# Kernel tuning notes

Measured on AMD Instinct MI355X. Metric: run time of the kernel, lower is better.

Reference implementation:

```python
import jax, jax.numpy as jnp
import numpy as np

POOLED = 7          # output_size
SCALE = 0.25        # spatial_scale
SRATIO = 2          # sampling_ratio (fixed in module)
IMG_H, IMG_W = 800.0, 1216.0


def setup_inputs() -> dict:
    key = jax.random.key(0)
    kf, kb, kx, ky, kw, kh = jax.random.split(key, 6)
    B, C, H, W = 2, 256, 200, 304
    features = jax.random.normal(kf, (B, C, H, W), dtype=jnp.float32)
    N = 1000
    bidx = jax.random.randint(kb, (N,), 0, B).astype(jnp.float32)
    x1 = jax.random.uniform(kx, (N,), minval=0.0, maxval=IMG_W - 32.0)
    y1 = jax.random.uniform(ky, (N,), minval=0.0, maxval=IMG_H - 32.0)
    bw = jax.random.uniform(kw, (N,), minval=16.0, maxval=256.0)
    bh = jax.random.uniform(kh, (N,), minval=16.0, maxval=256.0)
    x2 = jnp.minimum(x1 + bw, IMG_W)
    y2 = jnp.minimum(y1 + bh, IMG_H)
    rois = jnp.stack([bidx, x1, y1, x2, y2], axis=1).astype(jnp.float32)
    return {"features": features, "rois": rois}


def _axis_interp(c, size):
    """Per-axis bilinear prep, matching torchvision roi_align (aligned=False)."""
    valid = (c >= -1.0) & (c <= size)
    c = jnp.maximum(c, 0.0)
    lo = jnp.floor(c).astype(jnp.int32)
    at_edge = lo >= size - 1
    lo = jnp.minimum(lo, size - 1)
    hi = jnp.minimum(lo + 1, size - 1)
    c = jnp.where(at_edge, lo.astype(c.dtype), c)
    frac = c - lo.astype(c.dtype)
    return lo, hi, frac, valid


def reference(features, rois):
    B, C, H, W = features.shape
    N = rois.shape[0]
    P, s = POOLED, SRATIO
    Ps = P * s

    f = jnp.transpose(features, (0, 2, 3, 1))  # [B, H, W, C]
    b = rois[:, 0].astype(jnp.int32)
    x1 = rois[:, 1] * SCALE
    y1 = rois[:, 2] * SCALE
    x2 = rois[:, 3] * SCALE
    y2 = rois[:, 4] * SCALE
    roi_w = jnp.maximum(x2 - x1, 1.0)
    roi_h = jnp.maximum(y2 - y1, 1.0)
    bin_w = roi_w / P
    bin_h = roi_h / P

    # sample-point centers: ph*bin + (iy+0.5)*bin/s  ==  (idx+0.5)/s * bin
    off = (jnp.arange(Ps, dtype=jnp.float32) + 0.5) / s  # [Ps]
    ys = y1[:, None] + off[None, :] * bin_h[:, None]     # [N, Ps]
    xs = x1[:, None] + off[None, :] * bin_w[:, None]     # [N, Ps]

    yl, yh, ly, vy = _axis_interp(ys, H)
    xl, xh, lx, vx = _axis_interp(xs, W)
    hy, hx = 1.0 - ly, 1.0 - lx

    bb = b[:, None, None]
    YL, YH = yl[:, :, None], yh[:, :, None]
    XL, XH = xl[:, None, :], xh[:, None, :]
    # gathered corner values: [N, Ps, Ps, C]
    v11 = f[bb, YL, XL]
    v12 = f[bb, YL, XH]
    v21 = f[bb, YH, XL]
    v22 = f[bb, YH, XH]

    w11 = (hy[:, :, None] * hx[:, None, :])[..., None]
    w12 = (hy[:, :, None] * lx[:, None, :])[..., None]
    w21 = (ly[:, :, None] * hx[:, None, :])[..., None]
    w22 = (ly[:, :, None] * lx[:, None, :])[..., None]
    mask = (vy[:, :, None] & vx[:, None, :]).astype(f.dtype)[..., None]

    val = (w11 * v11 + w12 * v12 + w21 * v21 + w22 * v22) * mask  # [N,Ps,Ps,C]
    out = val.reshape(N, P, s, P, s, C).mean(axis=(2, 4))          # [N,P,P,C]
    return jnp.transpose(out, (0, 3, 1, 2))                        # [N,C,P,P]
```

## Files before the change

### kernel.cpp

```cpp
#include <hip/hip_runtime.h>
#include <hip/hip_fp16.h>

#define POOLED 7
#define PP 49
#define ROI_SCALE 0.25f
#define FH 200
#define FW 304
#define FHW 60800
#define FC 256

__global__ __launch_bounds__(256) void transpose_f16(
    const float* __restrict__ in, __half* __restrict__ out)
{
    __shared__ float tile[64][33];
    const int b   = blockIdx.z;
    const int hw0 = blockIdx.x * 32;
    const int c0  = blockIdx.y * 64;
    const int tx  = threadIdx.x;
    const int ty  = threadIdx.y;

    #pragma unroll
    for (int i = 0; i < 8; i++) {
        int c = c0 + ty + i * 8;
        tile[ty + i * 8][tx] = in[((size_t)b * FC + c) * FHW + hw0 + tx];
    }
    __syncthreads();
    #pragma unroll
    for (int i = 0; i < 4; i++) {
        int hwl = ty + i * 8;
        __half2 h = __floats2half2_rn(tile[2 * tx][hwl], tile[2 * tx + 1][hwl]);
        *reinterpret_cast<__half2*>(
            out + ((size_t)b * FHW + hw0 + hwl) * FC + c0 + 2 * tx) = h;
    }
}

__device__ __forceinline__ float4 ldpx(const __half* p) {
    uint2 u = *reinterpret_cast<const uint2*>(p);
    __half2 h0 = *reinterpret_cast<const __half2*>(&u.x);
    __half2 h1 = *reinterpret_cast<const __half2*>(&u.y);
    float2 f0 = __half22float2(h0);
    float2 f1 = __half22float2(h1);
    return make_float4(f0.x, f0.y, f1.x, f1.y);
}

__global__ __launch_bounds__(256) void roi_gather_f16(
    const __half* __restrict__ f,
    const float* __restrict__ rois,
    float* __restrict__ out)
{
    __shared__ float s_out[FC * 13];
    __shared__ int   s_ylo[14], s_yhi[14], s_xlo[14], s_xhi[14];
    __shared__ float s_ly[14], s_lx[14];
    __shared__ int   s_vy[14], s_vx[14];

    const int n    = blockIdx.x;
    const int q    = blockIdx.y;
    const int b0   = q * 13;
    const int nb   = (q == 3) ? 10 : 13;
    const int tid  = threadIdx.x;
    const int lane = tid & 63;
    const int wave = tid >> 6;

    const float* r = rois + (size_t)n * 5;
    const int   bi = (int)r[0];
    const float x1 = r[1] * ROI_SCALE;
    const float y1 = r[2] * ROI_SCALE;
    const float bin_w = fmaxf(r[3] * ROI_SCALE - x1, 1.0f) / (float)POOLED;
    const float bin_h = fmaxf(r[4] * ROI_SCALE - y1, 1.0f) / (float)POOLED;

    if (tid < 14) {
        float c = y1 + ((float)tid + 0.5f) * 0.5f * bin_h;
        int v = (c >= -1.0f) && (c <= (float)FH);
        c = fmaxf(c, 0.0f);
        int lo = (int)floorf(c);
        int edge = (lo >= FH - 1);
        lo = min(lo, FH - 1);
        s_yhi[tid] = min(lo + 1, FH - 1);
        s_ylo[tid] = lo;
        s_ly[tid]  = edge ? 0.0f : (c - (float)lo);
        s_vy[tid]  = v;
    } else if (tid >= 64 && tid < 78) {
        int j = tid - 64;
        float c = x1 + ((float)j + 0.5f) * 0.5f * bin_w;
        int v = (c >= -1.0f) && (c <= (float)FW);
        c = fmaxf(c, 0.0f);
        int lo = (int)floorf(c);
        int edge = (lo >= FW - 1);
        lo = min(lo, FW - 1);
        s_xhi[j] = min(lo + 1, FW - 1);
        s_xlo[j] = lo;
        s_lx[j]  = edge ? 0.0f : (c - (float)lo);
        s_vx[j]  = v;
    }
    __syncthreads();

    const __half* fb = f + (size_t)bi * (FHW * FC) + 4 * lane;

    for (int bin = b0 + wave; bin < b0 + nb; bin += 4) {
        int ph = bin / 7, pw = bin - ph * 7;
        float ax = 0.f, ay = 0.f, az = 0.f, aw = 0.f;
        #pragma unroll
        for (int iy = 0; iy < 2; iy++) {
            int   sy = 2 * ph + iy;
            int   rlo = s_ylo[sy] * FW, rhi = s_yhi[sy] * FW;
            float ly = s_ly[sy], hy = 1.0f - ly;
            float my = s_vy[sy] ? 1.0f : 0.0f;
            #pragma unroll
            for (int ix = 0; ix < 2; ix++) {
                int   sx = 2 * pw + ix;
                int   xlo = s_xlo[sx], xhi = s_xhi[sx];
                float lx = s_lx[sx], hx = 1.0f - lx;
                float m = s_vx[sx] ? my : 0.0f;
                float w11 = m * hy * hx, w12 = m * hy * lx;
                float w21 = m * ly * hx, w22 = m * ly * lx;
                float4 v11 = ldpx(fb + (size_t)(rlo + xlo) * FC);
                float4 v12 = ldpx(fb + (size_t)(rlo + xhi) * FC);
                float4 v21 = ldpx(fb + (size_t)(rhi + xlo) * FC);
                float4 v22 = ldpx(fb + (size_t)(rhi + xhi) * FC);
                ax += w11 * v11.x + w12 * v12.x + w21 * v21.x + w22 * v22.x;
                ay += w11 * v11.y + w12 * v12.y + w21 * v21.y + w22 * v22.y;
                az += w11 * v11.z + w12 * v12.z + w21 * v21.z + w22 * v22.z;
                aw += w11 * v11.w + w12 * v12.w + w21 * v21.w + w22 * v22.w;
            }
        }
        int c4 = 4 * lane, bl = bin - b0;
        s_out[(c4 + 0) * nb + bl] = ax * 0.25f;
        s_out[(c4 + 1) * nb + bl] = ay * 0.25f;
        s_out[(c4 + 2) * nb + bl] = az * 0.25f;
        s_out[(c4 + 3) * nb + bl] = aw * 0.25f;
    }
    __syncthreads();

    float* ob = out + (size_t)n * (FC * PP);
    int tot = FC * nb;
    for (int i = tid; i < tot; i += 256) {
        int c = i / nb, bl = i - c * nb;
        ob[c * PP + b0 + bl] = s_out[i];
    }
}

__global__ __launch_bounds__(256) void roi_align_fallback(
    const float* __restrict__ feat,
    const float* __restrict__ rois,
    float* __restrict__ out,
    int C, int H, int W, int N)
{
    int idx = blockIdx.x * blockDim.x + threadIdx.x;
    int total = N * C * PP;
    if (idx >= total) return;

    int pw = idx % POOLED;
    int ph = (idx / POOLED) % POOLED;
    int c  = (idx / PP) % C;
    int n  = idx / (PP * C);

    const float* r = rois + (size_t)n * 5;
    int   b  = (int)r[0];
    float x1 = r[1] * ROI_SCALE;
    float y1 = r[2] * ROI_SCALE;
    float bin_w = fmaxf(r[3] * ROI_SCALE - x1, 1.0f) / (float)POOLED;
    float bin_h = fmaxf(r[4] * ROI_SCALE - y1, 1.0f) / (float)POOLED;

    const float* fc = feat + ((size_t)b * C + c) * (size_t)(H * W);

    float acc = 0.0f;
    #pragma unroll
    for (int iy = 0; iy < 2; iy++) {
        float yy = y1 + ((float)(ph * 2 + iy) + 0.5f) * bin_h * 0.5f;
        bool  vy = (yy >= -1.0f) && (yy <= (float)H);
        float cy = fmaxf(yy, 0.0f);
        int   ylo = (int)floorf(cy);
        bool  ey = (ylo >= H - 1);
        ylo = min(ylo, H - 1);
        int   yhi = min(ylo + 1, H - 1);
        if (ey) cy = (float)ylo;
        float ly = cy - (float)ylo, hy = 1.0f - ly;

        #pragma unroll
        for (int ix = 0; ix < 2; ix++) {
            float xx = x1 + ((float)(pw * 2 + ix) + 0.5f) * bin_w * 0.5f;
            bool  vx = (xx >= -1.0f) && (xx <= (float)W);
            float cx = fmaxf(xx, 0.0f);
            int   xlo = (int)floorf(cx);
            bool  ex = (xlo >= W - 1);
            xlo = min(xlo, W - 1);
            int   xhi = min(xlo + 1, W - 1);
            if (ex) cx = (float)xlo;
            float lx = cx - (float)xlo, hx = 1.0f - lx;

            if (vy && vx) {
                float v11 = fc[(size_t)ylo * W + xlo];
                float v12 = fc[(size_t)ylo * W + xhi];
                float v21 = fc[(size_t)yhi * W + xlo];
                float v22 = fc[(size_t)yhi * W + xhi];
                acc += hy * (hx * v11 + lx * v12) + ly * (hx * v21 + lx * v22);
            }
        }
    }
    out[idx] = acc * 0.25f;
}

extern "C" void kernel_launch(void* const* d_in, const int* in_sizes, int n_in,
                              void* d_out, int out_size, void* d_ws, size_t ws_size,
                              hipStream_t stream) {
    const float* feat = (const float*)d_in[0];
    const float* rois = (const float*)d_in[1];
    float* out = (float*)d_out;

    const int N = in_sizes[1] / 5;
    const int B = in_sizes[0] / (FC * FHW);

    size_t need = (size_t)B * FHW * FC * sizeof(__half);
    if (ws_size >= need) {
        __half* f16 = (__half*)d_ws;
        transpose_f16<<<dim3(FHW / 32, FC / 64, B), dim3(32, 8), 0, stream>>>(feat, f16);
        roi_gather_f16<<<dim3(N, 4), 256, 0, stream>>>(f16, rois, out);
    } else {
        int total = N * FC * PP;
        roi_align_fallback<<<(total + 255) / 256, 256, 0, stream>>>(feat, rois, out, FC, FH, FW, N);
    }
}
```

Before: 93.63 us.

## Assign one bin per wave with half-wave corner split and 16-byte loads

The ROI gather kernel now launches 13 blocks per ROI, and each wave handles exactly one output bin. The two half-waves each load one x-corner (lo or hi) for all 256 channels using 16-byte fp16 loads, and their partial sums are combined with a cross-half shuffle. Interpolation indices are computed per wave in registers instead of being staged through shared memory, and the output goes through a small shared tile. This raises parallelism and memory-level concurrency, at the cost of more blocks, redundant per-ROI setup, and narrow strided output writes.

```diff
diff --git a/kernel.cpp b/kernel.cpp
--- a/kernel.cpp
+++ b/kernel.cpp
@@ -30,17 +30,19 @@
         int hwl = ty + i * 8;
         __half2 h = __floats2half2_rn(tile[2 * tx][hwl], tile[2 * tx + 1][hwl]);
         *reinterpret_cast<__half2*>(
-            out + ((size_t)b * FHW + hw0 + hwl) * FC + c0 + 2 * tx) = h;
-    }
-}
-
-__device__ __forceinline__ float4 ldpx(const __half* p) {
-    uint2 u = *reinterpret_cast<const uint2*>(p);
-    __half2 h0 = *reinterpret_cast<const __half2*>(&u.x);
-    __half2 h1 = *reinterpret_cast<const __half2*>(&u.y);
-    float2 f0 = __half22float2(h0);
-    float2 f1 = __half22float2(h1);
-    return make_float4(f0.x, f0.y, f1.x, f1.y);
+            out + ((size_t)b * FHW + hwl + hw0) * FC + c0 + 2 * tx) = h;
+    }
+}
+
+__device__ __forceinline__ void ld8(const __half* p, float o[8]) {
+    uint4 u = *reinterpret_cast<const uint4*>(p);
+    const __half2* h = reinterpret_cast<const __half2*>(&u);
+    #pragma unroll
+    for (int j = 0; j < 4; j++) {
+        float2 f = __half22float2(h[j]);
+        o[2 * j]     = f.x;
+        o[2 * j + 1] = f.y;
+    }
 }
 
 __global__ __launch_bounds__(256) void roi_gather_f16(
@@ -48,18 +50,15 @@
     const float* __restrict__ rois,
     float* __restrict__ out)
 {
-    __shared__ float s_out[FC * 13];
-    __shared__ int   s_ylo[14], s_yhi[14], s_xlo[14], s_xhi[14];
-    __shared__ float s_ly[14], s_lx[14];
-    __shared__ int   s_vy[14], s_vx[14];
+    __shared__ float s_out[4][260];
 
     const int n    = blockIdx.x;
     const int q    = blockIdx.y;
-    const int b0   = q * 13;
-    const int nb   = (q == 3) ? 10 : 13;
     const int tid  = threadIdx.x;
+    const int wave = tid >> 6;
     const int lane = tid & 63;
-    const int wave = tid >> 6;
+    const int hl   = lane & 31;
+    const bool hiHalf = lane >= 32;
 
     const float* r = rois + (size_t)n * 5;
     const int   bi = (int)r[0];
@@ -68,74 +67,78 @@
     const float bin_w = fmaxf(r[3] * ROI_SCALE - x1, 1.0f) / (float)POOLED;
     const float bin_h = fmaxf(r[4] * ROI_SCALE - y1, 1.0f) / (float)POOLED;
 
-    if (tid < 14) {
-        float c = y1 + ((float)tid + 0.5f) * 0.5f * bin_h;
-        int v = (c >= -1.0f) && (c <= (float)FH);
+    const int bin = min(4 * q + wave, 48);
+    const int ph = bin / 7;
+    const int pw = bin - ph * 7;
+
+    int rowlo[2], rowhi[2];
+    float why[2], wly[2];
+    #pragma unroll
+    for (int iy = 0; iy < 2; iy++) {
+        float c = y1 + ((float)(2 * ph + iy) + 0.5f) * 0.5f * bin_h;
+        float v = ((c >= -1.0f) && (c <= (float)FH)) ? 1.0f : 0.0f;
         c = fmaxf(c, 0.0f);
         int lo = (int)floorf(c);
-        int edge = (lo >= FH - 1);
+        bool edge = (lo >= FH - 1);
         lo = min(lo, FH - 1);
-        s_yhi[tid] = min(lo + 1, FH - 1);
-        s_ylo[tid] = lo;
-        s_ly[tid]  = edge ? 0.0f : (c - (float)lo);
-        s_vy[tid]  = v;
-    } else if (tid >= 64 && tid < 78) {
-        int j = tid - 64;
-        float c = x1 + ((float)j + 0.5f) * 0.5f * bin_w;
-        int v = (c >= -1.0f) && (c <= (float)FW);
+        rowlo[iy] = lo * FW;
+        rowhi[iy] = min(lo + 1, FH - 1) * FW;
+        float ly = edge ? 0.0f : (c - (float)lo);
+        why[iy] = v * (1.0f - ly);
+        wly[iy] = v * ly;
+    }
+    int   xoff[2];
+    float wx[2];
+    #pragma unroll
+    for (int ix = 0; ix < 2; ix++) {
+        float c = x1 + ((float)(2 * pw + ix) + 0.5f) * 0.5f * bin_w;
+        float v = ((c >= -1.0f) && (c <= (float)FW)) ? 1.0f : 0.0f;
         c = fmaxf(c, 0.0f);
         int lo = (int)floorf(c);
-        int edge = (lo >= FW - 1);
+        bool edge = (lo >= FW - 1);
         lo = min(lo, FW - 1);
-        s_xhi[j] = min(lo + 1, FW - 1);
-        s_xlo[j] = lo;
-        s_lx[j]  = edge ? 0.0f : (c - (float)lo);
-        s_vx[j]  = v;
+        int hi = min(lo + 1, FW - 1);
+        float lx = edge ? 0.0f : (c - (float)lo);
+        xoff[ix] = hiHalf ? hi : lo;
+        wx[ix]   = v * (hiHalf ? lx : (1.0f - lx));
+    }
+
+    const __half* base = f + (size_t)bi * (FHW * FC) + 8 * hl;
+
+    float acc[8] = {0.f, 0.f, 0.f, 0.f, 0.f, 0.f, 0.f, 0.f};
+    #pragma unroll
+    for (int iy = 0; iy < 2; iy++) {
+        #pragma unroll
+        for (int ix = 0; ix < 2; ix++) {
+            float vlo[8], vhi[8];
+            ld8(base + ((rowlo[iy] + xoff[ix]) << 8), vlo);
+            ld8(base + ((rowhi[iy] + xoff[ix]) << 8), vhi);
+            float wlo = why[iy] * wx[ix];
+            float whi = wly[iy] * wx[ix];
+            #pragma unroll
+            for (int k = 0; k < 8; k++)
+                acc[k] += wlo * vlo[k] + whi * vhi[k];
+        }
+    }
+
+    #pragma unroll
+    for (int k = 0; k < 8; k++)
+        acc[k] += __shfl_xor(acc[k], 32, 64);
+
+    const int bl = bin - 4 * q;
+    if (!hiHalf) {
+        #pragma unroll
+        for (int k = 0; k < 8; k++)
+            s_out[bl][8 * hl + k] = acc[k] * 0.25f;
     }
     __syncthreads();
 
-    const __half* fb = f + (size_t)bi * (FHW * FC) + 4 * lane;
-
-    for (int bin = b0 + wave; bin < b0 + nb; bin += 4) {
-        int ph = bin / 7, pw = bin - ph * 7;
-        float ax = 0.f, ay = 0.f, az = 0.f, aw = 0.f;
-        #pragma unroll
-        for (int iy = 0; iy < 2; iy++) {
-            int   sy = 2 * ph + iy;
-            int   rlo = s_ylo[sy] * FW, rhi = s_yhi[sy] * FW;
-            float ly = s_ly[sy], hy = 1.0f - ly;
-            float my = s_vy[sy] ? 1.0f : 0.0f;
-            #pragma unroll
-            for (int ix = 0; ix < 2; ix++) {
-                int   sx = 2 * pw + ix;
-                int   xlo = s_xlo[sx], xhi = s_xhi[sx];
-                float lx = s_lx[sx], hx = 1.0f - lx;
-                float m = s_vx[sx] ? my : 0.0f;
-                float w11 = m * hy * hx, w12 = m * hy * lx;
-                float w21 = m * ly * hx, w22 = m * ly * lx;
-                float4 v11 = ldpx(fb + (size_t)(rlo + xlo) * FC);
-                float4 v12 = ldpx(fb + (size_t)(rlo + xhi) * FC);
-                float4 v21 = ldpx(fb + (size_t)(rhi + xlo) * FC);
-                float4 v22 = ldpx(fb + (size_t)(rhi + xhi) * FC);
-                ax += w11 * v11.x + w12 * v12.x + w21 * v21.x + w22 * v22.x;
-                ay += w11 * v11.y + w12 * v12.y + w21 * v21.y + w22 * v22.y;
-                az += w11 * v11.z + w12 * v12.z + w21 * v21.z + w22 * v22.z;
-                aw += w11 * v11.w + w12 * v12.w + w21 * v21.w + w22 * v22.w;
-            }
-        }
-        int c4 = 4 * lane, bl = bin - b0;
-        s_out[(c4 + 0) * nb + bl] = ax * 0.25f;
-        s_out[(c4 + 1) * nb + bl] = ay * 0.25f;
-        s_out[(c4 + 2) * nb + bl] = az * 0.25f;
-        s_out[(c4 + 3) * nb + bl] = aw * 0.25f;
-    }
-    __syncthreads();
-
-    float* ob = out + (size_t)n * (FC * PP);
-    int tot = FC * nb;
-    for (int i = tid; i < tot; i += 256) {
-        int c = i / nb, bl = i - c * nb;
-        ob[c * PP + b0 + bl] = s_out[i];
+    const int nb = min(49 - 4 * q, 4);
+    float* ob = out + (size_t)n * (FC * PP) + 4 * q;
+    #pragma unroll
+    for (int b2 = 0; b2 < 4; b2++) {
+        if (b2 < nb)
+            ob[tid * PP + b2] = s_out[b2][tid];
     }
 }
 
@@ -214,7 +217,7 @@
     if (ws_size >= need) {
         __half* f16 = (__half*)d_ws;
         transpose_f16<<<dim3(FHW / 32, FC / 64, B), dim3(32, 8), 0, stream>>>(feat, f16);
-        roi_gather_f16<<<dim3(N, 4), 256, 0, stream>>>(f16, rois, out);
+        roi_gather_f16<<<dim3(N, 13), 256, 0, stream>>>(f16, rois, out);
     } else {
         int total = N * FC * PP;
         roi_align_fallback<<<(total + 255) / 256, 256, 0, stream>>>(feat, rois, out, FC, FH, FW, N);
```

Result: slower. 123.6 us (+32.0%).
